# Optimization experiments

Measured on AMD Instinct MI355X. Metric: run time of the kernel, lower is better.

Reference implementation:

```python
import jax, jax.numpy as jnp
import numpy as np

N0, N1, N2 = 100000, 50000, 8000   # src/dst node counts per block (dst = first n_dst of src)
E0, E1 = 600000, 80000             # edges per block
F_IN, HID, H, C = 256, 64, 4, 47   # in feats, hidden per head, heads, classes
NEG_SLOPE = 0.2


def setup_inputs() -> dict:
    key = jax.random.key(0)
    ks = jax.random.split(key, 12)
    rn = lambda k, shape, s=1.0: jax.random.normal(k, shape, jnp.float32) * s
    return {
        "x":   rn(ks[0], (N0, F_IN)),
        "W1":  rn(ks[1], (F_IN, H * HID), 0.05),
        "al1": rn(ks[2], (H, HID), 0.1),
        "ar1": rn(ks[3], (H, HID), 0.1),
        "b1":  jnp.zeros((H * HID,), jnp.float32),
        "W2":  rn(ks[4], (H * HID, H * C), 0.05),
        "al2": rn(ks[5], (H, C), 0.1),
        "ar2": rn(ks[6], (H, C), 0.1),
        "b2":  jnp.zeros((H * C,), jnp.float32),
        "src0": jax.random.randint(ks[7], (E0,), 0, N0, jnp.int32),
        "dst0": jax.random.randint(ks[8], (E0,), 0, N1, jnp.int32),
        "src1": jax.random.randint(ks[9], (E1,), 0, N1, jnp.int32),
        "dst1": jax.random.randint(ks[10], (E1,), 0, N2, jnp.int32),
    }


def gat_conv(h, src, dst, n_dst, W, attn_l, attn_r, bias):
    """DGL GATConv on a bipartite block: dst nodes = first n_dst src nodes."""
    nh, d = attn_l.shape
    feat = (h @ W).reshape(-1, nh, d)                     # [N_src, H, D]
    el = jnp.einsum('nhd,hd->nh', feat, attn_l)           # [N_src, H]
    er = jnp.einsum('nhd,hd->nh', feat[:n_dst], attn_r)   # [N_dst, H]
    e = jax.nn.leaky_relu(el[src] + er[dst], NEG_SLOPE)   # [E, H]
    # segment (edge) softmax over destination neighborhoods
    m = jax.ops.segment_max(e, dst, num_segments=n_dst)   # [N_dst, H]
    ee = jnp.exp(e - m[dst])
    s = jax.ops.segment_sum(ee, dst, num_segments=n_dst)
    alpha = ee / s[dst]                                   # [E, H]
    # scatter-weighted aggregation of source features
    out = jax.ops.segment_sum(alpha[:, :, None] * feat[src], dst, num_segments=n_dst)
    return out + bias.reshape(1, nh, d)                   # [N_dst, H, D]


def reference(x, W1, al1, ar1, b1, W2, al2, ar2, b2, src0, dst0, src1, dst1):
    h = gat_conv(x, src0, dst0, N1, W1, al1, ar1, b1)     # [N1, H, HID]
    h = jax.nn.elu(h).reshape(N1, -1)                     # activation + flatten heads
    h = gat_conv(h, src1, dst1, N2, W2, al2, ar2, b2)     # [N2, H, C], no activation on last layer
    return h.mean(axis=1)                                 # mean over heads -> [N2, C]
```

## Files before the change

kernel.cpp:

```cpp
#include <hip/hip_runtime.h>

#define CN0 100000
#define CN1 50000
#define CN2 8000
#define CE0 600000
#define CE1 80000
#define CFIN 256
#define CHID 64
#define CNH 4
#define CNC 47
#define CHD1 256
#define CHC2 188

static __host__ __device__ inline int cdiv(int a, int b) { return (a + b - 1) / b; }

typedef __bf16 bf16x8 __attribute__((ext_vector_type(8)));
typedef __bf16 bf16x4 __attribute__((ext_vector_type(4)));
typedef float f32x16 __attribute__((ext_vector_type(16)));

__global__ __launch_bounds__(256) void prep_w2_kernel(const float* __restrict__ W1,
                                                      __bf16* __restrict__ W1Th,
                                                      __bf16* __restrict__ W1Tl,
                                                      const float* __restrict__ W2,
                                                      __bf16* __restrict__ W2Th,
                                                      __bf16* __restrict__ W2Tl) {
    int id = blockIdx.x * 256 + threadIdx.x;
    const int tot1 = CHD1 * CFIN;
    if (id < tot1) {
        int n = id >> 8, k = id & 255;
        float w = W1[(size_t)k * CHD1 + n];
        __bf16 h = (__bf16)w;
        W1Th[id] = h;
        W1Tl[id] = (__bf16)(w - (float)h);
    } else {
        int id2 = id - tot1;
        if (id2 >= CHC2 * CHD1) return;
        int n = id2 >> 8, k = id2 & 255;
        float w = W2[(size_t)k * CHC2 + n];
        __bf16 h = (__bf16)w;
        W2Th[id2] = h;
        W2Tl[id2] = (__bf16)(w - (float)h);
    }
}

#define KP 40
template <bool ASPLIT>
__global__ __launch_bounds__(256) void gemm_mfma_kernel(const float* __restrict__ Af,
                                                        const __bf16* __restrict__ Ahp,
                                                        const __bf16* __restrict__ Alp,
                                                        const __bf16* __restrict__ BTh,
                                                        const __bf16* __restrict__ BTl,
                                                        float* __restrict__ C,
                                                        int M, int N, int K) {
    __shared__ __align__(16) __bf16 Ah[128 * KP];
    __shared__ __align__(16) __bf16 Al[128 * KP];
    __shared__ __align__(16) __bf16 Bh[128 * KP];
    __shared__ __align__(16) __bf16 Bl[128 * KP];
    int tid = threadIdx.x;
    int wave = tid >> 6, lane = tid & 63;
    int rowBase = blockIdx.x * 128, colBase = blockIdx.y * 128;
    int wr = wave >> 1, wc = wave & 1;

    f32x16 acc[2][2];
#pragma unroll
    for (int m = 0; m < 2; m++)
#pragma unroll
        for (int n = 0; n < 2; n++)
#pragma unroll
            for (int r = 0; r < 16; r++) acc[m][n][r] = 0.f;

    const int arow = tid >> 1;
    const int akc = (tid & 1) * 16;
    const int bcol = tid & 127;
    const int bsel = tid >> 7;
    const bool avalid = (rowBase + arow) < M;
    const int gcol = colBase + bcol;
    const bool bvalid = gcol < N;
    const float* aF = &Af[(size_t)(rowBase + arow) * K + akc];
    const __bf16* aH = &Ahp[(size_t)(rowBase + arow) * K + akc];
    const __bf16* aL = &Alp[(size_t)(rowBase + arow) * K + akc];
    const __bf16* bptr = (bsel ? BTl : BTh) + (size_t)gcol * K;
    __bf16* bdst = (bsel ? Bl : Bh) + bcol * KP;

    const int rc = lane & 31;
    const int kb = (lane >> 5) * 8;

    float4 pa[4];
    bf16x8 pah[2], pal[2];
    bf16x8 pb[4];

    auto LOAD = [&](int k0) {
        if constexpr (ASPLIT) {
#pragma unroll
            for (int c = 0; c < 4; c++)
                pa[c] = avalid ? *reinterpret_cast<const float4*>(aF + k0 + c * 4)
                               : make_float4(0.f, 0.f, 0.f, 0.f);
        } else {
            bf16x8 z = {};
            pah[0] = avalid ? *reinterpret_cast<const bf16x8*>(aH + k0) : z;
            pah[1] = avalid ? *reinterpret_cast<const bf16x8*>(aH + k0 + 8) : z;
            pal[0] = avalid ? *reinterpret_cast<const bf16x8*>(aL + k0) : z;
            pal[1] = avalid ? *reinterpret_cast<const bf16x8*>(aL + k0 + 8) : z;
        }
        bf16x8 z = {};
#pragma unroll
        for (int c = 0; c < 4; c++)
            pb[c] = bvalid ? *reinterpret_cast<const bf16x8*>(&bptr[k0 + c * 8]) : z;
    };

    auto STORE = [&]() {
        if constexpr (ASPLIT) {
#pragma unroll
            for (int c = 0; c < 4; c++) {
                float4 v = pa[c];
                __bf16 h0 = (__bf16)v.x, h1 = (__bf16)v.y, h2 = (__bf16)v.z, h3 = (__bf16)v.w;
                bf16x4 hv = {h0, h1, h2, h3};
                bf16x4 lv = {(__bf16)(v.x - (float)h0), (__bf16)(v.y - (float)h1),
                             (__bf16)(v.z - (float)h2), (__bf16)(v.w - (float)h3)};
                int o = arow * KP + akc + c * 4;
                *reinterpret_cast<bf16x4*>(&Ah[o]) = hv;
                *reinterpret_cast<bf16x4*>(&Al[o]) = lv;
            }
        } else {
            int o = arow * KP + akc;
            *reinterpret_cast<bf16x8*>(&Ah[o]) = pah[0];
            *reinterpret_cast<bf16x8*>(&Ah[o + 8]) = pah[1];
            *reinterpret_cast<bf16x8*>(&Al[o]) = pal[0];
            *reinterpret_cast<bf16x8*>(&Al[o + 8]) = pal[1];
        }
#pragma unroll
        for (int c = 0; c < 4; c++) *reinterpret_cast<bf16x8*>(&bdst[c * 8]) = pb[c];
    };

    const int nK = K >> 5;
    LOAD(0);
    for (int t = 0; t < nK; t++) {
        __syncthreads();
        STORE();
        __syncthreads();
        if (t + 1 < nK) LOAD((t + 1) * 32);

#pragma unroll
        for (int ks = 0; ks < 32; ks += 16) {
            bf16x8 fah[2], fal[2], fbh[2], fbl[2];
#pragma unroll
            for (int m = 0; m < 2; m++) {
                int r = wr * 64 + m * 32 + rc;
                fah[m] = *reinterpret_cast<const bf16x8*>(&Ah[r * KP + ks + kb]);
                fal[m] = *reinterpret_cast<const bf16x8*>(&Al[r * KP + ks + kb]);
            }
#pragma unroll
            for (int n = 0; n < 2; n++) {
                int cL = wc * 64 + n * 32 + rc;
                fbh[n] = *reinterpret_cast<const bf16x8*>(&Bh[cL * KP + ks + kb]);
                fbl[n] = *reinterpret_cast<const bf16x8*>(&Bl[cL * KP + ks + kb]);
            }
#pragma unroll
            for (int m = 0; m < 2; m++)
#pragma unroll
                for (int n = 0; n < 2; n++) {
                    acc[m][n] = __builtin_amdgcn_mfma_f32_32x32x16_bf16(fah[m], fbh[n],
                                                                        acc[m][n], 0, 0, 0);
                    acc[m][n] = __builtin_amdgcn_mfma_f32_32x32x16_bf16(fah[m], fbl[n],
                                                                        acc[m][n], 0, 0, 0);
                    acc[m][n] = __builtin_amdgcn_mfma_f32_32x32x16_bf16(fal[m], fbh[n],
                                                                        acc[m][n], 0, 0, 0);
                }
        }
    }

#pragma unroll
    for (int m = 0; m < 2; m++)
#pragma unroll
        for (int n = 0; n < 2; n++) {
            int col = colBase + wc * 64 + n * 32 + rc;
            if (col >= N) continue;
            int rbase = rowBase + wr * 64 + m * 32 + 4 * (lane >> 5);
#pragma unroll
            for (int r = 0; r < 16; r++) {
                int row = rbase + (r & 3) + 8 * (r >> 2);
                if (row < M) C[(size_t)row * N + col] = acc[m][n][r];
            }
        }
}

__global__ __launch_bounds__(256) void scores1_kernel(const float* __restrict__ feat,
                                                      const float* __restrict__ al,
                                                      const float* __restrict__ ar,
                                                      float* __restrict__ el,
                                                      float* __restrict__ er, int n_dst) {
    int n = blockIdx.x;
    int tid = threadIdx.x;
    int h = tid >> 6, dd = tid & 63;
    float f = feat[(size_t)n * CHD1 + tid];
    float pl = f * al[h * CHID + dd];
    float pr = f * ar[h * CHID + dd];
#pragma unroll
    for (int off = 32; off > 0; off >>= 1) {
        pl += __shfl_down(pl, off);
        pr += __shfl_down(pr, off);
    }
    if (dd == 0) {
        el[n * CNH + h] = pl;
        if (n < n_dst) er[n * CNH + h] = pr;
    }
}

__global__ __launch_bounds__(192) void scores2_kernel(const float* __restrict__ feat,
                                                      const float* __restrict__ al,
                                                      const float* __restrict__ ar,
                                                      float* __restrict__ el,
                                                      float* __restrict__ er, int n_dst) {
    int n = blockIdx.x;
    int tid = threadIdx.x;
    __shared__ float pl[CHC2], pr[CHC2];
    if (tid < CHC2) {
        float f = feat[(size_t)n * CHC2 + tid];
        pl[tid] = f * al[tid];
        pr[tid] = f * ar[tid];
    }
    __syncthreads();
    if (tid < CNH) {
        float sl = 0.f, sr = 0.f;
        for (int c = 0; c < CNC; c++) {
            sl += pl[tid * CNC + c];
            sr += pr[tid * CNC + c];
        }
        el[n * CNH + tid] = sl;
        if (n < n_dst) er[n * CNH + tid] = sr;
    }
}

__global__ void hist2_kernel(const int* __restrict__ dst0, int* __restrict__ cnt0,
                             const int* __restrict__ dst1, int* __restrict__ cnt1) {
    int i = blockIdx.x * blockDim.x + threadIdx.x;
    if (i < CE0) {
        atomicAdd(&cnt0[dst0[i]], 1);
    } else {
        int j = i - CE0;
        if (j < CE1) atomicAdd(&cnt1[dst1[j]], 1);
    }
}

__global__ __launch_bounds__(256) void scan1_kernel(const int* __restrict__ cnt0,
                                                    int* __restrict__ rp0, int* __restrict__ cur0,
                                                    int* __restrict__ bsums0, int nb0,
                                                    const int* __restrict__ cnt1,
                                                    int* __restrict__ rp1, int* __restrict__ cur1,
                                                    int* __restrict__ bsums1) {
    __shared__ int sm[256];
    int gb = blockIdx.x, tid = threadIdx.x;
    const int* cnt; int* rp; int* cur; int* bsums; int n; int b;
    if (gb < nb0) { cnt = cnt0; rp = rp0; cur = cur0; bsums = bsums0; n = CN1; b = gb; }
    else          { cnt = cnt1; rp = rp1; cur = cur1; bsums = bsums1; n = CN2; b = gb - nb0; }
    int base = b * 1024 + tid * 4;
    int v0 = 0, v1 = 0, v2 = 0, v3 = 0;
    if (base + 3 < n) {
        int4 q = *reinterpret_cast<const int4*>(&cnt[base]);
        v0 = q.x; v1 = q.y; v2 = q.z; v3 = q.w;
    } else {
        if (base + 0 < n) v0 = cnt[base + 0];
        if (base + 1 < n) v1 = cnt[base + 1];
        if (base + 2 < n) v2 = cnt[base + 2];
        if (base + 3 < n) v3 = cnt[base + 3];
    }
    int s1 = v0 + v1, s2 = s1 + v2, s3 = s2 + v3;
    sm[tid] = s3;
    __syncthreads();
    for (int off = 1; off < 256; off <<= 1) {
        int t = (tid >= off) ? sm[tid - off] : 0;
        __syncthreads();
        sm[tid] += t;
        __syncthreads();
    }
    int prefix = (tid > 0) ? sm[tid - 1] : 0;
    if (base + 0 < n) { rp[base + 1] = prefix + v0; cur[base + 0] = prefix; }
    if (base + 1 < n) { rp[base + 2] = prefix + s1; cur[base + 1] = prefix + v0; }
    if (base + 2 < n) { rp[base + 3] = prefix + s2; cur[base + 2] = prefix + s1; }
    if (base + 3 < n) { rp[base + 4] = prefix + s3; cur[base + 3] = prefix + s2; }
    if (tid == 255) bsums[b] = sm[255];
    if (b == 0 && tid == 0) rp[0] = 0;
}

__global__ __launch_bounds__(256) void scan2_kernel(int* __restrict__ bsums0, int nb0,
                                                    int* __restrict__ bsums1, int nb1) {
    __shared__ int sm[256];
    int tid = threadIdx.x;
    int* bsums = (blockIdx.x == 0) ? bsums0 : bsums1;
    int nb = (blockIdx.x == 0) ? nb0 : nb1;
    int v = (tid < nb) ? bsums[tid] : 0;
    sm[tid] = v;
    __syncthreads();
    for (int off = 1; off < 256; off <<= 1) {
        int t = (tid >= off) ? sm[tid - off] : 0;
        __syncthreads();
        sm[tid] += t;
        __syncthreads();
    }
    if (tid < nb) bsums[tid] = sm[tid] - v;
}

__global__ __launch_bounds__(256) void scan3_kernel(int* __restrict__ rp0, int* __restrict__ cur0,
                                                    const int* __restrict__ bsums0, int nb0,
                                                    int* __restrict__ rp1, int* __restrict__ cur1,
                                                    const int* __restrict__ bsums1) {
    int gb = blockIdx.x, tid = threadIdx.x;
    int* rp; int* cur; const int* bsums; int n; int b;
    if (gb < nb0) { rp = rp0; cur = cur0; bsums = bsums0; n = CN1; b = gb; }
    else          { rp = rp1; cur = cur1; bsums = bsums1; n = CN2; b = gb - nb0; }
    if (b == 0) return;
    int add = bsums[b];
    int idx = b * 1024 + tid * 4;
#pragma unroll
    for (int u = 0; u < 4; u++) {
        int p = idx + u;
        if (p < n) cur[p] += add;
        if (p + 1 <= n) rp[p + 1] += add;
    }
}

__global__ void scatter2_kernel(const int* __restrict__ dst0, const int* __restrict__ src0,
                                int* __restrict__ cur0, int* __restrict__ csr0,
                                const int* __restrict__ dst1, const int* __restrict__ src1,
                                int* __restrict__ cur1, int* __restrict__ csr1) {
    int i = blockIdx.x * blockDim.x + threadIdx.x;
    if (i < CE0) {
        int p = atomicAdd(&cur0[dst0[i]], 1);
        csr0[p] = src0[i];
    } else {
        int j = i - CE0;
        if (j < CE1) {
            int p = atomicAdd(&cur1[dst1[j]], 1);
            csr1[p] = src1[j];
        }
    }
}

__global__ __launch_bounds__(256) void alpha_kernel(const float* __restrict__ el,
                                                    const float* __restrict__ er,
                                                    const int* __restrict__ rp,
                                                    const int* __restrict__ csrsrc,
                                                    float* __restrict__ alpha, int n_dst) {
    int wid = (blockIdx.x * 256 + threadIdx.x) >> 6;
    int lane = threadIdx.x & 63;
    if (wid >= n_dst) return;
    int begin = rp[wid], end = rp[wid + 1];
    float4 erv = *reinterpret_cast<const float4*>(&er[wid * 4]);
    float m[4], s[4];
#pragma unroll
    for (int h = 0; h < 4; h++) { m[h] = -1e30f; s[h] = 0.f; }
    for (int i = begin + lane; i < end; i += 64) {
        int sn = csrsrc[i];
        float4 elv = *reinterpret_cast<const float4*>(&el[sn * 4]);
        float v[4] = {elv.x + erv.x, elv.y + erv.y, elv.z + erv.z, elv.w + erv.w};
#pragma unroll
        for (int h = 0; h < 4; h++) {
            float vv = v[h] > 0.f ? v[h] : 0.2f * v[h];
            float nm = fmaxf(m[h], vv);
            s[h] = s[h] * __expf(m[h] - nm) + __expf(vv - nm);
            m[h] = nm;
        }
    }
#pragma unroll
    for (int off = 1; off < 64; off <<= 1) {
#pragma unroll
        for (int h = 0; h < 4; h++) {
            float om = __shfl_xor(m[h], off);
            float os = __shfl_xor(s[h], off);
            float nm = fmaxf(m[h], om);
            s[h] = s[h] * __expf(m[h] - nm) + os * __expf(om - nm);
            m[h] = nm;
        }
    }
    float inv[4];
#pragma unroll
    for (int h = 0; h < 4; h++) inv[h] = s[h] > 0.f ? 1.f / s[h] : 0.f;
    for (int i = begin + lane; i < end; i += 64) {
        int sn = csrsrc[i];
        float4 elv = *reinterpret_cast<const float4*>(&el[sn * 4]);
        float v[4] = {elv.x + erv.x, elv.y + erv.y, elv.z + erv.z, elv.w + erv.w};
        float a[4];
#pragma unroll
        for (int h = 0; h < 4; h++) {
            float vv = v[h] > 0.f ? v[h] : 0.2f * v[h];
            a[h] = __expf(vv - m[h]) * inv[h];
        }
        *reinterpret_cast<float4*>(&alpha[(size_t)i * 4]) = make_float4(a[0], a[1], a[2], a[3]);
    }
}

#define CHUNK 128
__global__ __launch_bounds__(256) void agg1_kernel(const float* __restrict__ feat,
                                                   const float* __restrict__ alpha,
                                                   const int* __restrict__ rp,
                                                   const int* __restrict__ csrsrc,
                                                   const float* __restrict__ bias,
                                                   __bf16* __restrict__ h1h,
                                                   __bf16* __restrict__ h1l) {
    int dstn = blockIdx.x;
    int tid = threadIdx.x;
    int wave = tid >> 6, lane = tid & 63;
    __shared__ int s_src[CHUNK];
    __shared__ __align__(16) float s_alpha[CHUNK][4];
    __shared__ __align__(16) float s_red[3][256];
    int begin = rp[dstn], end = rp[dstn + 1];
    int head = lane >> 4;
    float4 acc = make_float4(0.f, 0.f, 0.f, 0.f);

    for (int cbase = begin; cbase < end; cbase += CHUNK) {
        int cn = min(end - cbase, CHUNK);
        for (int j = tid; j < cn; j += 256) {
            s_src[j] = csrsrc[cbase + j];
            *reinterpret_cast<float4*>(&s_alpha[j][0]) =
                *reinterpret_cast<const float4*>(&alpha[(size_t)(cbase + j) * 4]);
        }
        __syncthreads();
        for (int j = wave; j < cn; j += 4) {
            int sn = s_src[j];
            float a = s_alpha[j][head];
            float4 f = *reinterpret_cast<const float4*>(&feat[(size_t)sn * CHD1 + lane * 4]);
            acc.x += a * f.x; acc.y += a * f.y; acc.z += a * f.z; acc.w += a * f.w;
        }
        __syncthreads();
    }
    if (wave > 0) *reinterpret_cast<float4*>(&s_red[wave - 1][lane * 4]) = acc;
    __syncthreads();
    if (wave == 0) {
#pragma unroll
        for (int w = 0; w < 3; w++) {
            float4 o = *reinterpret_cast<float4*>(&s_red[w][lane * 4]);
            acc.x += o.x; acc.y += o.y; acc.z += o.z; acc.w += o.w;
        }
        float4 b = *reinterpret_cast<const float4*>(&bias[lane * 4]);
        float r[4] = {acc.x + b.x, acc.y + b.y, acc.z + b.z, acc.w + b.w};
        bf16x4 hv, lv;
#pragma unroll
        for (int u = 0; u < 4; u++) {
            float e = r[u] > 0.f ? r[u] : expm1f(r[u]);
            __bf16 h = (__bf16)e;
            hv[u] = h;
            lv[u] = (__bf16)(e - (float)h);
        }
        *reinterpret_cast<bf16x4*>(&h1h[(size_t)dstn * CHD1 + lane * 4]) = hv;
        *reinterpret_cast<bf16x4*>(&h1l[(size_t)dstn * CHD1 + lane * 4]) = lv;
    }
}

__global__ __launch_bounds__(256) void agg2_kernel(const float* __restrict__ feat,
                                                   const float* __restrict__ alpha,
                                                   const int* __restrict__ rp,
                                                   const int* __restrict__ csrsrc,
                                                   const float* __restrict__ bias,
                                                   float* __restrict__ out) {
    int dstn = blockIdx.x;
    int tid = threadIdx.x;
    int wave = tid >> 6, lane = tid & 63;
    __shared__ int s_src[CHUNK];
    __shared__ __align__(16) float s_alpha[CHUNK][4];
    __shared__ float s_red[3][192];
    __shared__ float s_out[192];
    int begin = rp[dstn], end = rp[dstn + 1];
    int f0 = lane, f1 = lane + 64, f2 = lane + 128;
    int h0 = f0 / CNC, h1_ = f1 / CNC, h2 = f2 < CHC2 ? f2 / CNC : 3;
    float a0c = 0.f, a1c = 0.f, a2c = 0.f;

    for (int cbase = begin; cbase < end; cbase += CHUNK) {
        int cn = min(end - cbase, CHUNK);
        for (int j = tid; j < cn; j += 256) {
            s_src[j] = csrsrc[cbase + j];
            *reinterpret_cast<float4*>(&s_alpha[j][0]) =
                *reinterpret_cast<const float4*>(&alpha[(size_t)(cbase + j) * 4]);
        }
        __syncthreads();
        for (int j = wave; j < cn; j += 4) {
            int sn = s_src[j];
            const float* fr = &feat[(size_t)sn * CHC2];
            a0c += s_alpha[j][h0] * fr[f0];
            a1c += s_alpha[j][h1_] * fr[f1];
            if (f2 < CHC2) a2c += s_alpha[j][h2] * fr[f2];
        }
        __syncthreads();
    }
    if (wave > 0) {
        s_red[wave - 1][f0] = a0c;
        s_red[wave - 1][f1] = a1c;
        if (f2 < 192) s_red[wave - 1][f2] = a2c;
    }
    __syncthreads();
    if (wave == 0) {
#pragma unroll
        for (int w = 0; w < 3; w++) {
            a0c += s_red[w][f0];
            a1c += s_red[w][f1];
            if (f2 < 192) a2c += s_red[w][f2];
        }
        s_out[f0] = a0c + bias[f0];
        if (f1 < CHC2) s_out[f1] = a1c + bias[f1];
        if (f2 < CHC2) s_out[f2] = a2c + bias[f2];
    }
    __syncthreads();
    if (tid < CNC) {
        out[(size_t)dstn * CNC + tid] =
            0.25f * (s_out[tid] + s_out[CNC + tid] + s_out[2 * CNC + tid] + s_out[3 * CNC + tid]);
    }
}

extern "C" void kernel_launch(void* const* d_in, const int* in_sizes, int n_in,
                              void* d_out, int out_size, void* d_ws, size_t ws_size,
                              hipStream_t stream) {
    const float* x   = (const float*)d_in[0];
    const float* W1  = (const float*)d_in[1];
    const float* al1 = (const float*)d_in[2];
    const float* ar1 = (const float*)d_in[3];
    const float* b1  = (const float*)d_in[4];
    const float* W2  = (const float*)d_in[5];
    const float* al2 = (const float*)d_in[6];
    const float* ar2 = (const float*)d_in[7];
    const float* b2  = (const float*)d_in[8];
    const int* src0  = (const int*)d_in[9];
    const int* dst0  = (const int*)d_in[10];
    const int* src1  = (const int*)d_in[11];
    const int* dst1  = (const int*)d_in[12];
    float* out = (float*)d_out;

    char* base = (char*)d_ws;
    size_t off = 0;
    auto carve = [&](size_t bytes) {
        void* p = base + off;
        off = (off + bytes + 255) & ~(size_t)255;
        return p;
    };
    float* feat1   = (float*)carve((size_t)CN0 * CHD1 * 4);
    __bf16* h1h    = (__bf16*)carve((size_t)CN1 * CHD1 * 2);
    __bf16* h1l    = (__bf16*)carve((size_t)CN1 * CHD1 * 2);
    float* el1     = (float*)carve((size_t)CN0 * CNH * 4);
    float* er1     = (float*)carve((size_t)CN1 * CNH * 4);
    int* rp0       = (int*)carve((CN1 + 1) * 4);
    int* cnt0      = (int*)carve(CN1 * 4);
    int* cnt1      = (int*)carve(CN2 * 4);
    int* csrsrc0   = (int*)carve((size_t)CE0 * 4);
    float* alpha0  = (float*)carve((size_t)CE0 * CNH * 4);
    int* rp1       = (int*)carve((CN2 + 1) * 4);
    int* csrsrc1   = (int*)carve((size_t)CE1 * 4);
    float* alpha1  = (float*)carve((size_t)CE1 * CNH * 4);
    int* bsums0    = (int*)carve(64 * 4);
    int* bsums1    = (int*)carve(64 * 4);
    __bf16* W1Th   = (__bf16*)carve((size_t)CHD1 * CFIN * 2);
    __bf16* W1Tl   = (__bf16*)carve((size_t)CHD1 * CFIN * 2);
    __bf16* W2Th   = (__bf16*)carve((size_t)CHC2 * CHD1 * 2);
    __bf16* W2Tl   = (__bf16*)carve((size_t)CHC2 * CHD1 * 2);
    float* feat2 = feat1;
    float* el2 = el1;
    float* er2 = er1;

    prep_w2_kernel<<<cdiv(CHD1 * CFIN + CHC2 * CHD1, 256), 256, 0, stream>>>(
        W1, W1Th, W1Tl, W2, W2Th, W2Tl);

    hipMemsetAsync(cnt0, 0, (size_t)(CN1 + CN2 + 64) * 4, stream);
    hist2_kernel<<<cdiv(CE0 + CE1, 256), 256, 0, stream>>>(dst0, cnt0, dst1, cnt1);
    int nb0 = cdiv(CN1, 1024), nb1 = cdiv(CN2, 1024);
    scan1_kernel<<<nb0 + nb1, 256, 0, stream>>>(cnt0, rp0, cnt0, bsums0, nb0,
                                                cnt1, rp1, cnt1, bsums1);
    scan2_kernel<<<2, 256, 0, stream>>>(bsums0, nb0, bsums1, nb1);
    scan3_kernel<<<nb0 + nb1, 256, 0, stream>>>(rp0, cnt0, bsums0, nb0, rp1, cnt1, bsums1);
    scatter2_kernel<<<cdiv(CE0 + CE1, 256), 256, 0, stream>>>(dst0, src0, cnt0, csrsrc0,
                                                              dst1, src1, cnt1, csrsrc1);

    gemm_mfma_kernel<true><<<dim3(cdiv(CN0, 128), cdiv(CHD1, 128)), 256, 0, stream>>>(
        x, nullptr, nullptr, W1Th, W1Tl, feat1, CN0, CHD1, CFIN);
    scores1_kernel<<<CN0, 256, 0, stream>>>(feat1, al1, ar1, el1, er1, CN1);
    alpha_kernel<<<cdiv(CN1, 4), 256, 0, stream>>>(el1, er1, rp0, csrsrc0, alpha0, CN1);
    agg1_kernel<<<CN1, 256, 0, stream>>>(feat1, alpha0, rp0, csrsrc0, b1, h1h, h1l);

    gemm_mfma_kernel<false><<<dim3(cdiv(CN1, 128), cdiv(CHC2, 128)), 256, 0, stream>>>(
        nullptr, h1h, h1l, W2Th, W2Tl, feat2, CN1, CHC2, CHD1);
    scores2_kernel<<<CN1, 192, 0, stream>>>(feat2, al2, ar2, el2, er2, CN2);
    alpha_kernel<<<cdiv(CN2, 4), 256, 0, stream>>>(el2, er2, rp1, csrsrc1, alpha1, CN2);
    agg2_kernel<<<CN2, 256, 0, stream>>>(feat2, alpha1, rp1, csrsrc1, b2, out);
}
```

Baseline: 552.1 us.

## Fuse layer-1 attention scores into GEMM epilogue and double-buffer LDS tiles

Computes the layer-1 el/er attention dot products inside the GEMM epilogue from accumulator registers, using cross-lane shuffles, and drops the separate scores1 kernel. That kernel re-read the 100k x 256 feature matrix. The GEMM also gets double-buffered dynamic shared memory, so the next tile is stored while the current one is consumed, leaving one barrier per K step instead of two. In exchange, LDS use doubles to 80 KB per block, which may lower occupancy, and the epilogue adds shuffle work.

```diff
diff --git a/kernel.cpp b/kernel.cpp
--- a/kernel.cpp
+++ b/kernel.cpp
@@ -44,18 +44,20 @@
 }
 
 #define KP 40
-template <bool ASPLIT>
+template <bool ASPLIT, bool SCORES>
 __global__ __launch_bounds__(256) void gemm_mfma_kernel(const float* __restrict__ Af,
                                                         const __bf16* __restrict__ Ahp,
                                                         const __bf16* __restrict__ Alp,
                                                         const __bf16* __restrict__ BTh,
                                                         const __bf16* __restrict__ BTl,
                                                         float* __restrict__ C,
-                                                        int M, int N, int K) {
-    __shared__ __align__(16) __bf16 Ah[128 * KP];
-    __shared__ __align__(16) __bf16 Al[128 * KP];
-    __shared__ __align__(16) __bf16 Bh[128 * KP];
-    __shared__ __align__(16) __bf16 Bl[128 * KP];
+                                                        int M, int N, int K,
+                                                        const float* __restrict__ al,
+                                                        const float* __restrict__ ar,
+                                                        float* __restrict__ el,
+                                                        float* __restrict__ er, int n_dst) {
+    extern __shared__ __align__(16) __bf16 smem[];
+    const int SZE = 128 * KP;
     int tid = threadIdx.x;
     int wave = tid >> 6, lane = tid & 63;
     int rowBase = blockIdx.x * 128, colBase = blockIdx.y * 128;
@@ -80,7 +82,6 @@
     const __bf16* aH = &Ahp[(size_t)(rowBase + arow) * K + akc];
     const __bf16* aL = &Alp[(size_t)(rowBase + arow) * K + akc];
     const __bf16* bptr = (bsel ? BTl : BTh) + (size_t)gcol * K;
-    __bf16* bdst = (bsel ? Bl : Bh) + bcol * KP;
 
     const int rc = lane & 31;
     const int kb = (lane >> 5) * 8;
@@ -108,7 +109,10 @@
             pb[c] = bvalid ? *reinterpret_cast<const bf16x8*>(&bptr[k0 + c * 8]) : z;
     };
 
-    auto STORE = [&]() {
+    auto STORE = [&](int buf) {
+        __bf16* Ah = smem + (0 + buf) * SZE;
+        __bf16* Al = smem + (2 + buf) * SZE;
+        __bf16* Bdst = smem + ((bsel ? 6 : 4) + buf) * SZE + bcol * KP;
         if constexpr (ASPLIT) {
 #pragma unroll
             for (int c = 0; c < 4; c++) {
@@ -129,17 +133,22 @@
             *reinterpret_cast<bf16x8*>(&Al[o + 8]) = pal[1];
         }
 #pragma unroll
-        for (int c = 0; c < 4; c++) *reinterpret_cast<bf16x8*>(&bdst[c * 8]) = pb[c];
+        for (int c = 0; c < 4; c++) *reinterpret_cast<bf16x8*>(&Bdst[c * 8]) = pb[c];
     };
 
     const int nK = K >> 5;
     LOAD(0);
+    STORE(0);
+    __syncthreads();
+    int cur = 0;
+
     for (int t = 0; t < nK; t++) {
-        __syncthreads();
-        STORE();
-        __syncthreads();
         if (t + 1 < nK) LOAD((t + 1) * 32);
 
+        const __bf16* Ah = smem + (0 + cur) * SZE;
+        const __bf16* Al = smem + (2 + cur) * SZE;
+        const __bf16* Bh = smem + (4 + cur) * SZE;
+        const __bf16* Bl = smem + (6 + cur) * SZE;
 #pragma unroll
         for (int ks = 0; ks < 32; ks += 16) {
             bf16x8 fah[2], fal[2], fbh[2], fbl[2];
@@ -167,6 +176,36 @@
                                                                         acc[m][n], 0, 0, 0);
                 }
         }
+        if (t + 1 < nK) STORE(cur ^ 1);
+        __syncthreads();
+        cur ^= 1;
+    }
+
+    if constexpr (SCORES) {
+        int head = (colBase >> 6) + wc;
+        float wa0 = al[head * 64 + rc], wa1 = al[head * 64 + 32 + rc];
+        float wr0 = ar[head * 64 + rc], wr1 = ar[head * 64 + 32 + rc];
+        int hi = lane >> 5;
+#pragma unroll
+        for (int m = 0; m < 2; m++) {
+#pragma unroll
+            for (int r = 0; r < 16; r++) {
+                float vl = acc[m][0][r] * wa0 + acc[m][1][r] * wa1;
+                float vr = acc[m][0][r] * wr0 + acc[m][1][r] * wr1;
+#pragma unroll
+                for (int off = 16; off > 0; off >>= 1) {
+                    vl += __shfl_xor(vl, off);
+                    vr += __shfl_xor(vr, off);
+                }
+                if (rc == 0) {
+                    int row = rowBase + wr * 64 + m * 32 + 4 * hi + (r & 3) + 8 * (r >> 2);
+                    if (row < M) {
+                        el[row * CNH + head] = vl;
+                        if (row < n_dst) er[row * CNH + head] = vr;
+                    }
+                }
+            }
+        }
     }
 
 #pragma unroll
@@ -182,28 +221,6 @@
                 if (row < M) C[(size_t)row * N + col] = acc[m][n][r];
             }
         }
-}
-
-__global__ __launch_bounds__(256) void scores1_kernel(const float* __restrict__ feat,
-                                                      const float* __restrict__ al,
-                                                      const float* __restrict__ ar,
-                                                      float* __restrict__ el,
-                                                      float* __restrict__ er, int n_dst) {
-    int n = blockIdx.x;
-    int tid = threadIdx.x;
-    int h = tid >> 6, dd = tid & 63;
-    float f = feat[(size_t)n * CHD1 + tid];
-    float pl = f * al[h * CHID + dd];
-    float pr = f * ar[h * CHID + dd];
-#pragma unroll
-    for (int off = 32; off > 0; off >>= 1) {
-        pl += __shfl_down(pl, off);
-        pr += __shfl_down(pr, off);
-    }
-    if (dd == 0) {
-        el[n * CNH + h] = pl;
-        if (n < n_dst) er[n * CNH + h] = pr;
-    }
 }
 
 __global__ __launch_bounds__(192) void scores2_kernel(const float* __restrict__ feat,
@@ -553,6 +570,12 @@
     float* el2 = el1;
     float* er2 = er1;
 
+    const int LDS_BYTES = 2 * 4 * 128 * KP * 2;
+    hipFuncSetAttribute((const void*)gemm_mfma_kernel<true, true>,
+                        hipFuncAttributeMaxDynamicSharedMemorySize, LDS_BYTES);
+    hipFuncSetAttribute((const void*)gemm_mfma_kernel<false, false>,
+                        hipFuncAttributeMaxDynamicSharedMemorySize, LDS_BYTES);
+
     prep_w2_kernel<<<cdiv(CHD1 * CFIN + CHC2 * CHD1, 256), 256, 0, stream>>>(
         W1, W1Th, W1Tl, W2, W2Th, W2Tl);
 
@@ -566,14 +589,16 @@
     scatter2_kernel<<<cdiv(CE0 + CE1, 256), 256, 0, stream>>>(dst0, src0, cnt0, csrsrc0,
                                                               dst1, src1, cnt1, csrsrc1);
 
-    gemm_mfma_kernel<true><<<dim3(cdiv(CN0, 128), cdiv(CHD1, 128)), 256, 0, stream>>>(
-        x, nullptr, nullptr, W1Th, W1Tl, feat1, CN0, CHD1, CFIN);
-    scores1_kernel<<<CN0, 256, 0, stream>>>(feat1, al1, ar1, el1, er1, CN1);
+    gemm_mfma_kernel<true, true><<<dim3(cdiv(CN0, 128), cdiv(CHD1, 128)), 256, LDS_BYTES,
+                                   stream>>>(x, nullptr, nullptr, W1Th, W1Tl, feat1,
+                                             CN0, CHD1, CFIN, al1, ar1, el1, er1, CN1);
     alpha_kernel<<<cdiv(CN1, 4), 256, 0, stream>>>(el1, er1, rp0, csrsrc0, alpha0, CN1);
     agg1_kernel<<<CN1, 256, 0, stream>>>(feat1, alpha0, rp0, csrsrc0, b1, h1h, h1l);
 
-    gemm_mfma_kernel<false><<<dim3(cdiv(CN1, 128), cdiv(CHC2, 128)), 256, 0, stream>>>(
-        nullptr, h1h, h1l, W2Th, W2Tl, feat2, CN1, CHC2, CHD1);
+    gemm_mfma_kernel<false, false><<<dim3(cdiv(CN1, 128), cdiv(CHC2, 128)), 256, LDS_BYTES,
+                                     stream>>>(nullptr, h1h, h1l, W2Th, W2Tl, feat2,
+                                               CN1, CHC2, CHD1, nullptr, nullptr,
+                                               nullptr, nullptr, 0);
     scores2_kernel<<<CN1, 192, 0, stream>>>(feat2, al2, ar2, el2, er2, CN2);
     alpha_kernel<<<cdiv(CN2, 4), 256, 0, stream>>>(el2, er2, rp1, csrsrc1, alpha1, CN2);
     agg2_kernel<<<CN2, 256, 0, stream>>>(feat2, alpha1, rp1, csrsrc1, b2, out);
```

After: 533.1 us. -3.5%, faster.
